# Performance work log

Measured on AMD Instinct MI355X. Metric: run time of the kernel, lower is better.

## Reference

```python
import jax, jax.numpy as jnp
import numpy as np

N, D_IN, D_HID, S = 50000, 128, 128, 25
BN_EPS = 1e-5
NORM_EPS = 1e-6


def setup_inputs() -> dict:
    key = jax.random.key(0)
    ks = jax.random.split(key, 16)

    def lin(k, fan_in, shape):
        b = 1.0 / np.sqrt(fan_in)
        return jax.random.uniform(k, shape, jnp.float32, -b, b)

    return {
        "features": jax.random.normal(ks[0], (N, D_IN), jnp.float32),
        "neigh_idx1": jax.random.randint(ks[1], (N, S), 0, N, jnp.int32),
        "neigh_idx2": jax.random.randint(ks[2], (N, S), 0, N, jnp.int32),
        # aggregator1: Linear(input_dim, input_dim)
        "agg1_W": lin(ks[3], D_IN, (D_IN, D_IN)),
        "agg1_b": lin(ks[4], D_IN, (D_IN,)),
        # fc1: Linear(2*input_dim, hidden_dim)
        "fc1_W": lin(ks[5], 2 * D_IN, (2 * D_IN, D_HID)),
        "fc1_b": lin(ks[6], 2 * D_IN, (D_HID,)),
        # aggregator2: Linear(hidden_dim, hidden_dim)
        "agg2_W": lin(ks[7], D_HID, (D_HID, D_HID)),
        "agg2_b": lin(ks[8], D_HID, (D_HID,)),
        # fc2: Linear(2*hidden_dim, hidden_dim)
        "fc2_W": lin(ks[9], 2 * D_HID, (2 * D_HID, D_HID)),
        "fc2_b": lin(ks[10], 2 * D_HID, (D_HID,)),
        # BatchNorm1d(hidden_dim)
        "bn_gamma": jnp.ones((D_HID,), jnp.float32),
        "bn_beta": jnp.zeros((D_HID,), jnp.float32),
    }


def _maxpool_agg(x, neigh_idx, W, b):
    # MaxPoolAggregator: relu(Linear(neighbor feats)) then max over sampled
    # neighbors. Transform once on all nodes, then gather -> max (same math,
    # avoids redundant per-neighbor GEMM work).
    h = jax.nn.relu(x @ W + b)              # [N, d_out]
    return jnp.max(h[neigh_idx], axis=1)    # [N, S, d_out] -> [N, d_out]


def reference(features, neigh_idx1, neigh_idx2,
              agg1_W, agg1_b, fc1_W, fc1_b,
              agg2_W, agg2_b, fc2_W, fc2_b,
              bn_gamma, bn_beta):
    # ---- layer 1 ----
    agg = _maxpool_agg(features, neigh_idx1, agg1_W, agg1_b)
    x = jnp.concatenate([features, agg], axis=1) @ fc1_W + fc1_b
    x = jax.nn.relu(x)
    # BatchNorm1d (training-mode batch statistics)
    mean = jnp.mean(x, axis=0)
    var = jnp.var(x, axis=0)
    x = (x - mean) * jax.lax.rsqrt(var + BN_EPS) * bn_gamma + bn_beta
    # dropout is identity in eval
    x = x / (jnp.linalg.norm(x, axis=1, keepdims=True) + NORM_EPS)
    # ---- layer 2 ----
    agg2 = _maxpool_agg(x, neigh_idx2, agg2_W, agg2_b)
    out = jnp.concatenate([x, agg2], axis=1) @ fc2_W + fc2_b
    return out
```

## Files before the change

kernel.cpp:

```cpp
#include <hip/hip_runtime.h>
#include <stdint.h>

typedef __attribute__((ext_vector_type(8))) short bf16x8;
typedef __attribute__((ext_vector_type(8))) unsigned short u16x8;
typedef __attribute__((ext_vector_type(4))) float f32x4;
typedef int int4a __attribute__((ext_vector_type(4), aligned(4)));

__device__ __forceinline__ float bf2f(uint16_t h) { return __uint_as_float(((uint32_t)h) << 16); }
__device__ __forceinline__ uint16_t f2bf(float f) {
  uint32_t u = __float_as_uint(f);
  u += 0x7fffu + ((u >> 16) & 1u);
  return (uint16_t)(u >> 16);
}

#define NSHADOW 64

__global__ __launch_bounds__(256) void prep_k(
    const float* __restrict__ W1, const float* __restrict__ Wf1,
    const float* __restrict__ W2, const float* __restrict__ Wf2,
    const float* __restrict__ b1, const float* __restrict__ bf1,
    const float* __restrict__ b2, const float* __restrict__ bf2,
    const float* __restrict__ gam, const float* __restrict__ bet,
    uint16_t* __restrict__ F1, uint16_t* __restrict__ Ff1,
    uint16_t* __restrict__ F2, uint16_t* __restrict__ Ff2,
    float* __restrict__ fb, float* __restrict__ fgb,
    float* __restrict__ shadow)
{
  int t = blockIdx.x * 256 + threadIdx.x;
  for (int i = t; i < NSHADOW * 256; i += 12288) shadow[i] = 0.f;
  {
    const float* W; uint16_t* D; int KTl; int g;
    if (t < 2048)      { W = W1;  D = F1;  KTl = 4; g = t; }
    else if (t < 6144) { W = Wf1; D = Ff1; KTl = 8; g = t - 2048; }
    else if (t < 8192) { W = W2;  D = F2;  KTl = 4; g = t - 6144; }
    else               { W = Wf2; D = Ff2; KTl = 8; g = t - 8192; }
    int c = g >> 6, l = g & 63;
    int tt = c / KTl, kk = c - tt * KTl;
    int m = l & 15, q = l >> 4;
    int n  = tt * 16 + m;
    int k0 = kk * 32 + q * 8;
    bf16x8 a;
#pragma unroll
    for (int j = 0; j < 8; j++) a[j] = (short)f2bf(W[(size_t)(k0 + j) * 128 + n]);
    *(bf16x8*)(D + (size_t)g * 8) = a;
  }
  if (blockIdx.x == 0) {
    int i = threadIdx.x;
    for (int j = i; j < 512; j += 256) {
      const float* src = (j < 128) ? b1 : (j < 256) ? bf1 : (j < 384) ? b2 : bf2;
      fb[j] = src[j & 127];
    }
    fgb[i] = (i < 128) ? gam[i] : bet[i & 127];
  }
}

template<int MODE>
__global__ __launch_bounds__(256) void gemm_l(
    const void* __restrict__ Av, const uint16_t* __restrict__ Wf,
    const float* __restrict__ bias, const float* __restrict__ scsh,
    uint16_t* __restrict__ D, uint16_t* __restrict__ XOUT, int M)
{
  const int lane = threadIdx.x & 63;
  const int wv   = threadIdx.x >> 6;
  const int row0 = blockIdx.x * 64 + wv * 16;
  if (row0 >= M) return;
  const int m = lane & 15, quad = lane >> 4;
  const int arow = row0 + m;

  bf16x8 afr[4];
  if (MODE == 1) {
    const float* A = (const float*)Av;
#pragma unroll
    for (int kk = 0; kk < 4; kk++) {
      const float* p = A + (size_t)arow * 128 + kk * 32 + quad * 8;
      f32x4 f0 = *(const f32x4*)p;
      f32x4 f1 = *(const f32x4*)(p + 4);
      bf16x8 a;
      a[0] = (short)f2bf(f0[0]); a[1] = (short)f2bf(f0[1]);
      a[2] = (short)f2bf(f0[2]); a[3] = (short)f2bf(f0[3]);
      a[4] = (short)f2bf(f1[0]); a[5] = (short)f2bf(f1[1]);
      a[6] = (short)f2bf(f1[2]); a[7] = (short)f2bf(f1[3]);
      afr[kk] = a;
    }
  } else {
    const uint16_t* A = (const uint16_t*)Av;
    float xv[32];
    float ss = 0.f;
#pragma unroll
    for (int kk = 0; kk < 4; kk++) {
      const int k0 = kk * 32 + quad * 8;
      bf16x8 y8 = *(const bf16x8*)(A + (size_t)arow * 128 + k0);
      f32x4 sc0 = *(const f32x4*)(scsh + k0);
      f32x4 sc1 = *(const f32x4*)(scsh + k0 + 4);
      f32x4 sh0 = *(const f32x4*)(scsh + 128 + k0);
      f32x4 sh1 = *(const f32x4*)(scsh + 128 + k0 + 4);
#pragma unroll
      for (int j = 0; j < 4; j++) {
        float a = bf2f((uint16_t)y8[j])     * sc0[j] + sh0[j];
        float b = bf2f((uint16_t)y8[4 + j]) * sc1[j] + sh1[j];
        xv[kk * 8 + j] = a; xv[kk * 8 + 4 + j] = b;
        ss += a * a + b * b;
      }
    }
    ss += __shfl_xor(ss, 16); ss += __shfl_xor(ss, 32);
    float inv = 1.0f / (sqrtf(ss) + 1e-6f);
#pragma unroll
    for (int kk = 0; kk < 4; kk++) {
      bf16x8 a;
#pragma unroll
      for (int j = 0; j < 8; j++) a[j] = (short)f2bf(xv[kk * 8 + j] * inv);
      afr[kk] = a;
    }
  }
#pragma unroll
  for (int kk = 0; kk < 4; kk++)
    *(bf16x8*)(XOUT + (size_t)arow * 128 + kk * 32 + quad * 8) = afr[kk];

#pragma unroll
  for (int tt = 0; tt < 8; tt++) {
    bf16x8 bfr[4];
#pragma unroll
    for (int kk = 0; kk < 4; kk++)
      bfr[kk] = *(const bf16x8*)(Wf + ((size_t)(tt * 4 + kk) * 64 + lane) * 8);
    f32x4 acc = {0.f, 0.f, 0.f, 0.f};
#pragma unroll
    for (int kk = 0; kk < 4; kk++)
      acc = __builtin_amdgcn_mfma_f32_16x16x32_bf16(afr[kk], bfr[kk], acc, 0, 0, 0);
    const int col = tt * 16 + m;
    const float bv = bias[col];
#pragma unroll
    for (int r = 0; r < 4; r++) {
      float v = fmaxf(acc[r] + bv, 0.f);
      D[(size_t)(row0 + quad * 4 + r) * 128 + col] = f2bf(v);
    }
  }
}

template<bool STATS, int ODT>
__global__ __launch_bounds__(256, 3) void gemm_g(
    const uint16_t* __restrict__ A0, const uint16_t* __restrict__ H,
    const int* __restrict__ idx, const uint16_t* __restrict__ Wf,
    const float* __restrict__ bias, void* __restrict__ Dv,
    float* __restrict__ shadow, int M)
{
  __shared__ __align__(16) uint16_t agg[16 * 136];
  const int lane = threadIdx.x & 63;
  const int wv   = threadIdx.x >> 6;
  const int row0 = blockIdx.x * 16;
  if (row0 >= M) return;
  const int m = lane & 15, quad = lane >> 4;
  const int arow = row0 + m;

  bf16x8 afr[8];
#pragma unroll
  for (int kk = 0; kk < 4; kk++)
    afr[kk] = *(const bf16x8*)(A0 + (size_t)arow * 128 + kk * 32 + quad * 8);

  {
    const int rw = row0 + wv * 4 + quad;
    const int* ir = idx + (size_t)rw * 25;
    int ii[25];
#pragma unroll
    for (int b = 0; b < 6; b++) {
      int4a t4 = *(const int4a*)(ir + b * 4);
      ii[b * 4 + 0] = t4[0]; ii[b * 4 + 1] = t4[1];
      ii[b * 4 + 2] = t4[2]; ii[b * 4 + 3] = t4[3];
    }
    ii[24] = ir[24];
    u16x8 v[25];
#pragma unroll
    for (int e = 0; e < 25; e++) {
      uint32_t j = (uint32_t)ii[e];
      if (j >= (uint32_t)M) j = 0;
      v[e] = *(const u16x8*)(H + (size_t)j * 128 + m * 8);
    }
    __builtin_amdgcn_sched_barrier(0);
    u16x8 mx = v[0];
#pragma unroll
    for (int e = 1; e < 25; e++) {
#pragma unroll
      for (int x = 0; x < 8; x++) mx[x] = (v[e][x] > mx[x]) ? v[e][x] : mx[x];
    }
    *(u16x8*)(&agg[(wv * 4 + quad) * 136 + m * 8]) = mx;
  }
  __syncthreads();

#pragma unroll
  for (int kk = 0; kk < 4; kk++)
    afr[4 + kk] = *(const bf16x8*)(&agg[m * 136 + kk * 32 + quad * 8]);

#pragma unroll
  for (int t2 = 0; t2 < 2; t2++) {
    const int tt = wv * 2 + t2;
    bf16x8 bfr[8];
#pragma unroll
    for (int kk = 0; kk < 8; kk++)
      bfr[kk] = *(const bf16x8*)(Wf + ((size_t)(tt * 8 + kk) * 64 + lane) * 8);
    f32x4 acc = {0.f, 0.f, 0.f, 0.f};
#pragma unroll
    for (int kk = 0; kk < 8; kk++)
      acc = __builtin_amdgcn_mfma_f32_16x16x32_bf16(afr[kk], bfr[kk], acc, 0, 0, 0);

    const int col = tt * 16 + m;
    const float bv = bias[col];
    float vals[4];
#pragma unroll
    for (int r = 0; r < 4; r++) {
      float v = acc[r] + bv;
      if (STATS) v = fmaxf(v, 0.f);
      vals[r] = v;
      size_t oidx = (size_t)(row0 + quad * 4 + r) * 128 + col;
      if (ODT == 0) ((uint16_t*)Dv)[oidx] = f2bf(v);
      else          ((float*)Dv)[oidx] = v;
    }
    if (STATS) {
      float s = vals[0] + vals[1] + vals[2] + vals[3];
      float q = vals[0]*vals[0] + vals[1]*vals[1] + vals[2]*vals[2] + vals[3]*vals[3];
      s += __shfl_xor(s, 16); s += __shfl_xor(s, 32);
      q += __shfl_xor(q, 16); q += __shfl_xor(q, 32);
      if (quad == 0) {
        float* slot = shadow + (size_t)(blockIdx.x & (NSHADOW - 1)) * 256;
        atomicAdd(&slot[col], s);
        atomicAdd(&slot[128 + col], q);
      }
    }
  }
}

__global__ __launch_bounds__(256) void bn_fin_k(
    const float* __restrict__ shadow, const float* __restrict__ fgb,
    float* __restrict__ scsh, int M)
{
  __shared__ float ps[256], pq[256];
  const int tid = threadIdx.x;
  const int col = tid & 127, part = tid >> 7;
  float s = 0.f, q = 0.f;
#pragma unroll 8
  for (int sl = part * 32; sl < part * 32 + 32; sl++) {
    s += shadow[sl * 256 + col];
    q += shadow[sl * 256 + 128 + col];
  }
  ps[tid] = s; pq[tid] = q;
  __syncthreads();
  if (tid < 128) {
    s = ps[tid] + ps[tid + 128];
    q = pq[tid] + pq[tid + 128];
    float invN = 1.0f / (float)M;
    float mean = s * invN;
    float var  = fmaxf(q * invN - mean * mean, 0.f);
    float g = fgb[tid] * rsqrtf(var + 1e-5f);
    scsh[tid] = g;
    scsh[128 + tid] = fgb[128 + tid] - mean * g;
  }
}

extern "C" void kernel_launch(void* const* d_in, const int* in_sizes, int n_in,
                              void* d_out, int out_size, void* d_ws, size_t ws_size,
                              hipStream_t stream)
{
  const float* features = (const float*)d_in[0];
  const int*   idx1     = (const int*)d_in[1];
  const int*   idx2     = (const int*)d_in[2];
  const float* agg1_W   = (const float*)d_in[3];
  const float* agg1_b   = (const float*)d_in[4];
  const float* fc1_W    = (const float*)d_in[5];
  const float* fc1_b    = (const float*)d_in[6];
  const float* agg2_W   = (const float*)d_in[7];
  const float* agg2_b   = (const float*)d_in[8];
  const float* fc2_W    = (const float*)d_in[9];
  const float* fc2_b    = (const float*)d_in[10];
  const float* bn_g     = (const float*)d_in[11];
  const float* bn_b     = (const float*)d_in[12];

  const int N = in_sizes[0] / 128;

  char* w = (char*)d_ws;
  float* shadow = (float*)w; w += NSHADOW * 256 * 4;
  uint16_t* F1  = (uint16_t*)w; w += 128 * 128 * 2;
  uint16_t* Ff1 = (uint16_t*)w; w += 128 * 256 * 2;
  uint16_t* F2  = (uint16_t*)w; w += 128 * 128 * 2;
  uint16_t* Ff2 = (uint16_t*)w; w += 128 * 256 * 2;
  float* fb   = (float*)w; w += 512 * 4;
  float* fgb  = (float*)w; w += 256 * 4;
  float* scsh = (float*)w; w += 256 * 4;
  size_t NB = (size_t)N * 128 * 2;
  uint16_t* Xb = (uint16_t*)w; w += NB;
  uint16_t* h1 = (uint16_t*)w; w += NB;
  uint16_t* yb = (uint16_t*)w; w += NB;
  uint16_t* xb = (uint16_t*)w; w += NB;
  uint16_t* h2 = (uint16_t*)w; w += NB;

  const int tb  = (N + 15) / 16;
  const int tbl = (N + 63) / 64;

  prep_k<<<48, 256, 0, stream>>>(agg1_W, fc1_W, agg2_W, fc2_W,
      agg1_b, fc1_b, agg2_b, fc2_b, bn_g, bn_b,
      F1, Ff1, F2, Ff2, fb, fgb, shadow);
  gemm_l<1><<<tbl, 256, 0, stream>>>(features, F1, fb + 0, nullptr, h1, Xb, N);
  gemm_g<true, 0><<<tb, 256, 0, stream>>>(Xb, h1, idx1, Ff1, fb + 128, yb, shadow, N);
  bn_fin_k<<<1, 256, 0, stream>>>(shadow, fgb, scsh, N);
  gemm_l<2><<<tbl, 256, 0, stream>>>(yb, F2, fb + 256, scsh, h2, xb, N);
  gemm_g<false, 1><<<tb, 256, 0, stream>>>(xb, h2, idx2, Ff2, fb + 384, d_out, nullptr, N);

  (void)n_in; (void)out_size; (void)ws_size;
}
```

Before: 212.4 us.

## Use nontemporal loads/stores, inline-asm SGPR-base gathers, and vector max

```diff
diff --git a/kernel.cpp b/kernel.cpp
--- a/kernel.cpp
+++ b/kernel.cpp
@@ -73,8 +73,8 @@
 #pragma unroll
     for (int kk = 0; kk < 4; kk++) {
       const float* p = A + (size_t)arow * 128 + kk * 32 + quad * 8;
-      f32x4 f0 = *(const f32x4*)p;
-      f32x4 f1 = *(const f32x4*)(p + 4);
+      f32x4 f0 = __builtin_nontemporal_load((const f32x4*)p);
+      f32x4 f1 = __builtin_nontemporal_load((const f32x4*)(p + 4));
       bf16x8 a;
       a[0] = (short)f2bf(f0[0]); a[1] = (short)f2bf(f0[1]);
       a[2] = (short)f2bf(f0[2]); a[3] = (short)f2bf(f0[3]);
@@ -89,7 +89,7 @@
 #pragma unroll
     for (int kk = 0; kk < 4; kk++) {
       const int k0 = kk * 32 + quad * 8;
-      bf16x8 y8 = *(const bf16x8*)(A + (size_t)arow * 128 + k0);
+      bf16x8 y8 = __builtin_nontemporal_load((const bf16x8*)(A + (size_t)arow * 128 + k0));
       f32x4 sc0 = *(const f32x4*)(scsh + k0);
       f32x4 sc1 = *(const f32x4*)(scsh + k0 + 4);
       f32x4 sh0 = *(const f32x4*)(scsh + 128 + k0);
@@ -114,7 +114,8 @@
   }
 #pragma unroll
   for (int kk = 0; kk < 4; kk++)
-    *(bf16x8*)(XOUT + (size_t)arow * 128 + kk * 32 + quad * 8) = afr[kk];
+    __builtin_nontemporal_store(afr[kk],
+        (bf16x8*)(XOUT + (size_t)arow * 128 + kk * 32 + quad * 8));
 
 #pragma unroll
   for (int tt = 0; tt < 8; tt++) {
@@ -131,13 +132,14 @@
 #pragma unroll
     for (int r = 0; r < 4; r++) {
       float v = fmaxf(acc[r] + bv, 0.f);
-      D[(size_t)(row0 + quad * 4 + r) * 128 + col] = f2bf(v);
+      __builtin_nontemporal_store(f2bf(v),
+          &D[(size_t)(row0 + quad * 4 + r) * 128 + col]);
     }
   }
 }
 
 template<bool STATS, int ODT>
-__global__ __launch_bounds__(256, 3) void gemm_g(
+__global__ __launch_bounds__(256) void gemm_g(
     const uint16_t* __restrict__ A0, const uint16_t* __restrict__ H,
     const int* __restrict__ idx, const uint16_t* __restrict__ Wf,
     const float* __restrict__ bias, void* __restrict__ Dv,
@@ -154,33 +156,41 @@
   bf16x8 afr[8];
 #pragma unroll
   for (int kk = 0; kk < 4; kk++)
-    afr[kk] = *(const bf16x8*)(A0 + (size_t)arow * 128 + kk * 32 + quad * 8);
+    afr[kk] = __builtin_nontemporal_load(
+        (const bf16x8*)(A0 + (size_t)arow * 128 + kk * 32 + quad * 8));
 
   {
     const int rw = row0 + wv * 4 + quad;
     const int* ir = idx + (size_t)rw * 25;
-    int ii[25];
-#pragma unroll
-    for (int b = 0; b < 6; b++) {
-      int4a t4 = *(const int4a*)(ir + b * 4);
-      ii[b * 4 + 0] = t4[0]; ii[b * 4 + 1] = t4[1];
-      ii[b * 4 + 2] = t4[2]; ii[b * 4 + 3] = t4[3];
-    }
-    ii[24] = ir[24];
+    uint32_t vo[25];
+    {
+      int ii[25];
+#pragma unroll
+      for (int b = 0; b < 6; b++) {
+        int4a t4 = __builtin_nontemporal_load((const int4a*)(ir + b * 4));
+        ii[b * 4 + 0] = t4[0]; ii[b * 4 + 1] = t4[1];
+        ii[b * 4 + 2] = t4[2]; ii[b * 4 + 3] = t4[3];
+      }
+      ii[24] = __builtin_nontemporal_load(ir + 24);
+#pragma unroll
+      for (int e = 0; e < 25; e++) {
+        uint32_t j = (uint32_t)ii[e];
+        if (j >= (uint32_t)M) j = 0;
+        vo[e] = j * 256u + (uint32_t)(m * 16);
+      }
+    }
     u16x8 v[25];
 #pragma unroll
-    for (int e = 0; e < 25; e++) {
-      uint32_t j = (uint32_t)ii[e];
-      if (j >= (uint32_t)M) j = 0;
-      v[e] = *(const u16x8*)(H + (size_t)j * 128 + m * 8);
-    }
+    for (int e = 0; e < 25; e++)
+      asm volatile("global_load_dwordx4 %0, %1, %2"
+                   : "=v"(v[e]) : "v"(vo[e]), "s"(H));
+    asm volatile("s_waitcnt vmcnt(0)" ::: "memory");
     __builtin_amdgcn_sched_barrier(0);
+#pragma unroll
+    for (int e = 0; e < 25; e++) asm volatile("" : "+v"(v[e]));
     u16x8 mx = v[0];
 #pragma unroll
-    for (int e = 1; e < 25; e++) {
-#pragma unroll
-      for (int x = 0; x < 8; x++) mx[x] = (v[e][x] > mx[x]) ? v[e][x] : mx[x];
-    }
+    for (int e = 1; e < 25; e++) mx = __builtin_elementwise_max(mx, v[e]);
     *(u16x8*)(&agg[(wv * 4 + quad) * 136 + m * 8]) = mx;
   }
   __syncthreads();
@@ -210,8 +220,8 @@
       if (STATS) v = fmaxf(v, 0.f);
       vals[r] = v;
       size_t oidx = (size_t)(row0 + quad * 4 + r) * 128 + col;
-      if (ODT == 0) ((uint16_t*)Dv)[oidx] = f2bf(v);
-      else          ((float*)Dv)[oidx] = v;
+      if (ODT == 0) __builtin_nontemporal_store(f2bf(v), (uint16_t*)Dv + oidx);
+      else          __builtin_nontemporal_store(v, (float*)Dv + oidx);
     }
     if (STATS) {
       float s = vals[0] + vals[1] + vals[2] + vals[3];
```

Result: slower. 233.2 us (+9.8%).
